# Performance work log

Measured on AMD Instinct MI355X. Metric: run time of the kernel, lower is better.

The kernel has to match this reference:

```python
import jax, jax.numpy as jnp
import numpy as np

N = 50000        # nodes
E = 1600000      # edges (before self loops)
IN = 128         # in_channels
HID = 32         # hidden_channels
HEADS = 4
OUT = 16         # out_channels
B = 512          # graphs in batch
NEG_SLOPE = 0.2  # PyG GATConv default


def _uniform(key, shape, fan_in):
    s = 1.0 / np.sqrt(fan_in)
    return jax.random.uniform(key, shape, jnp.float32, -s, s)


def setup_inputs() -> dict:
    key = jax.random.key(0)
    ks = jax.random.split(key, 12)
    x = jax.random.normal(ks[0], (N, IN), jnp.float32)
    edge_index = jax.random.randint(ks[1], (2, E), 0, N, dtype=jnp.int64)
    batch = jnp.sort(jax.random.randint(ks[2], (N,), 0, B, dtype=jnp.int64))
    return {
        "x": x,
        "edge_index": edge_index,
        "batch": batch,
        "W1": _uniform(ks[3], (IN, HEADS * HID), IN),
        "att_src": _uniform(ks[4], (HEADS, HID), HID),
        "att_dst": _uniform(ks[5], (HEADS, HID), HID),
        "b1": jnp.zeros((HEADS * HID,), jnp.float32),
        "lin1_w": _uniform(ks[6], (HEADS * HID, HID), HEADS * HID),
        "lin1_b": _uniform(ks[7], (HID,), HEADS * HID),
        "lin2_w": _uniform(ks[8], (HID, OUT), HID),
        "lin2_b": _uniform(ks[9], (OUT,), HID),
    }


def _gat_conv(x, src, dst, W1, att_src, att_dst, b1):
    # h: [N, H, C]
    h = (x @ W1).reshape(N, HEADS, HID)
    a_s = (h * att_src).sum(-1)   # [N, H]
    a_d = (h * att_dst).sum(-1)   # [N, H]
    # per-edge attention logits [E', H]
    alpha = jax.nn.leaky_relu(a_s[src] + a_d[dst], negative_slope=NEG_SLOPE)
    # segment softmax over incoming edges of each destination node
    amax = jax.lax.stop_gradient(jax.ops.segment_max(alpha, dst, num_segments=N))
    ex = jnp.exp(alpha - amax[dst])
    den = jax.ops.segment_sum(ex, dst, num_segments=N)
    a = ex / (den[dst] + 1e-16)
    # weighted scatter-aggregate of source features: [N, H, C]
    out = jax.ops.segment_sum(h[src] * a[:, :, None], dst, num_segments=N)
    return out.reshape(N, HEADS * HID) + b1


def reference(x, edge_index, batch, W1, att_src, att_dst, b1, lin1_w, lin1_b, lin2_w, lin2_b):
    # add self loops (PyG GATConv default add_self_loops=True)
    loop = jnp.arange(N, dtype=edge_index.dtype)
    src = jnp.concatenate([edge_index[0], loop])
    dst = jnp.concatenate([edge_index[1], loop])
    # dropout layers are identity in eval mode
    xh = jax.nn.elu(_gat_conv(x, src, dst, W1, att_src, att_dst, b1))
    g = jax.ops.segment_sum(xh, batch, num_segments=B)  # global_add_pool -> [B, H*C]
    g = g @ lin1_w + lin1_b
    return g @ lin2_w + lin2_b
```

## Files before the change

### kernel.cpp

```cpp
#include <hip/hip_runtime.h>
#include <hip/hip_bf16.h>
#include <hip/hip_fp16.h>

#define N_NODES 50000
#define E_EDGES 1600000
#define IN_CH 128
#define HID 32
#define HEADS 4
#define HC (HEADS * HID)
#define OUT_CH 16
#define B_GRAPHS 512
#define NEG_SLOPE 0.2f
#define CAP 96
#define NB 256
#define BNODES 196
#define PCAP 7168
#define ACHUNK 4096
#define APART 391
#define ROWS_PB 64
#define GEMM_BLOCKS 782

__device__ __forceinline__ unsigned short f2bf(float f) {
    unsigned int u = __float_as_uint(f);
    unsigned int r = (u + 0x7FFFu + ((u >> 16) & 1u)) >> 16;
    return (unsigned short)r;
}

__device__ __forceinline__ float lrelu_exp(float v) {
    v = v > 0.f ? v : NEG_SLOPE * v;
    return __expf(v);
}

__global__ __launch_bounds__(256) void k_fused(const float* __restrict__ x,
                                               const float* __restrict__ W1,
                                               const float* __restrict__ att_src,
                                               const float* __restrict__ att_dst,
                                               const int* __restrict__ ei,
                                               unsigned short* __restrict__ hb,
                                               float* __restrict__ a_s,
                                               float* __restrict__ a_d,
                                               int* __restrict__ gcur,
                                               unsigned int* __restrict__ ebuf,
                                               float* __restrict__ g) {
    __shared__ float smem[12288];
    const int t = threadIdx.x;

    if (blockIdx.x < APART) {
        int* scnt = (int*)smem;
        int* sbase = scnt + 4 * NB;
        const int wv = t >> 6;
        const int e0 = blockIdx.x * ACHUNK;
        int e1 = e0 + ACHUNK; if (e1 > E_EDGES) e1 = E_EDGES;
        for (int i = t; i < 4 * NB; i += 256) scnt[i] = 0;
        __syncthreads();
        const int* __restrict__ dstp = ei + E_EDGES;
        for (int e = e0 + t; e < e1; e += 256) {
            int d = dstp[e];
            atomicAdd(&scnt[wv * NB + d / BNODES], 1);
        }
        __syncthreads();
        if (t < NB) {
            int c0 = scnt[0 * NB + t], c1 = scnt[1 * NB + t];
            int c2 = scnt[2 * NB + t], c3 = scnt[3 * NB + t];
            int base = atomicAdd(&gcur[t], c0 + c1 + c2 + c3);
            sbase[0 * NB + t] = base;
            sbase[1 * NB + t] = base + c0;
            sbase[2 * NB + t] = base + c0 + c1;
            sbase[3 * NB + t] = base + c0 + c1 + c2;
            scnt[0 * NB + t] = 0; scnt[1 * NB + t] = 0;
            scnt[2 * NB + t] = 0; scnt[3 * NB + t] = 0;
        }
        __syncthreads();
        for (int e = e0 + t; e < e1; e += 256) {
            int d = dstp[e];
            int s = ei[e];
            int b = d / BNODES;
            int dl = d - b * BNODES;
            int pos = sbase[wv * NB + b] + atomicAdd(&scnt[wv * NB + b], 1);
            if (pos < PCAP)
                ebuf[(size_t)b * PCAP + pos] = ((unsigned int)dl << 16) | (unsigned int)s;
        }
        return;
    }

    float* sX = smem;
    float* sW = smem + 8192;
    const int bid = blockIdx.x - APART;
    const int n0 = bid * ROWS_PB;

    int gt = bid * 256 + t;
    if (gt < B_GRAPHS * HC) g[gt] = 0.f;

    for (int i = t; i < ROWS_PB * 32; i += 256) {
        int r = i >> 5, c4 = i & 31;
        int n = n0 + r;
        float4 v = (n < N_NODES) ? ((const float4*)x)[(size_t)n * 32 + c4]
                                 : make_float4(0.f, 0.f, 0.f, 0.f);
        ((float4*)sX)[i] = v;
    }

    float acc[8][4];
#pragma unroll
    for (int j = 0; j < 8; j++)
#pragma unroll
        for (int c = 0; c < 4; c++) acc[j][c] = 0.f;

    const int tx = t & 31;
    const int ty = t >> 5;

    for (int kb = 0; kb < 4; kb++) {
        __syncthreads();
        for (int i = t; i < 32 * 32; i += 256) {
            ((float4*)sW)[i] =
                ((const float4*)W1)[(size_t)(kb * 32 + (i >> 5)) * 32 + (i & 31)];
        }
        __syncthreads();
#pragma unroll
        for (int kk = 0; kk < 32; kk += 4) {
            float4 w0 = *(float4*)&sW[(kk + 0) * 128 + tx * 4];
            float4 w1 = *(float4*)&sW[(kk + 1) * 128 + tx * 4];
            float4 w2 = *(float4*)&sW[(kk + 2) * 128 + tx * 4];
            float4 w3 = *(float4*)&sW[(kk + 3) * 128 + tx * 4];
#pragma unroll
            for (int j = 0; j < 8; j++) {
                float4 xv = *(float4*)&sX[(ty * 8 + j) * 128 + kb * 32 + kk];
                acc[j][0] += xv.x * w0.x + xv.y * w1.x + xv.z * w2.x + xv.w * w3.x;
                acc[j][1] += xv.x * w0.y + xv.y * w1.y + xv.z * w2.y + xv.w * w3.y;
                acc[j][2] += xv.x * w0.z + xv.y * w1.z + xv.z * w2.z + xv.w * w3.z;
                acc[j][3] += xv.x * w0.w + xv.y * w1.w + xv.z * w2.w + xv.w * w3.w;
            }
        }
    }

#pragma unroll
    for (int j = 0; j < 8; j++) {
        int n = n0 + ty * 8 + j;
        if (n < N_NODES) {
            ushort4 o;
            o.x = f2bf(acc[j][0]); o.y = f2bf(acc[j][1]);
            o.z = f2bf(acc[j][2]); o.w = f2bf(acc[j][3]);
            *(ushort4*)&hb[(size_t)n * HC + tx * 4] = o;
        }
    }

    __syncthreads();
    float* sH = smem;
#pragma unroll
    for (int j = 0; j < 8; j++) {
        float* row = &sH[(ty * 8 + j) * 129 + tx * 4];
        row[0] = acc[j][0]; row[1] = acc[j][1];
        row[2] = acc[j][2]; row[3] = acc[j][3];
    }
    __syncthreads();
    if (t < 128) {
        int r = t & 63;
        int n = n0 + r;
        const float* __restrict__ av = (t < 64) ? att_src : att_dst;
        float s0 = 0.f, s1 = 0.f, s2 = 0.f, s3 = 0.f;
#pragma unroll 4
        for (int j = 0; j < 32; j++) {
            const float* row = &sH[r * 129 + j];
            s0 += row[0]  * av[j];
            s1 += row[32] * av[32 + j];
            s2 += row[64] * av[64 + j];
            s3 += row[96] * av[96 + j];
        }
        if (n < N_NODES) {
            float* dst = (t < 64) ? a_s : a_d;
            *(float4*)(dst + (size_t)n * 4) = make_float4(s0, s1, s2, s3);
        }
    }
}

#define NPW 13
__global__ __launch_bounds__(1024) void k_aggB(const unsigned int* __restrict__ ebuf,
                                               const int* __restrict__ gcur,
                                               const float* __restrict__ a_s,
                                               const float* __restrict__ a_d,
                                               const unsigned short* __restrict__ hb,
                                               const float* __restrict__ b1,
                                               const int* __restrict__ batch,
                                               float* __restrict__ g) {
    __shared__ unsigned short sbuf[BNODES * CAP];
    __shared__ int scnt[BNODES];
    __shared__ float sWt[16][4][97];
    const int t = threadIdx.x;
    const int b = blockIdx.x;
    const int dbase = b * BNODES;

    for (int i = t; i < BNODES; i += 1024) {
        int d = dbase + i;
        scnt[i] = (d < N_NODES) ? 1 : 0;
        sbuf[i * CAP] = (unsigned short)d;
    }
    __syncthreads();
    int m = gcur[b]; if (m > PCAP) m = PCAP;
    for (int i = t; i < m; i += 1024) {
        unsigned int p = ebuf[(size_t)b * PCAP + i];
        int dl = p >> 16;
        int s = p & 0xFFFFu;
        int c = atomicAdd(&scnt[dl], 1);
        if (c < CAP) sbuf[dl * CAP + c] = (unsigned short)s;
    }
    __syncthreads();

    const int wv = t >> 6;
    const int l = t & 63;
    const int head = l >> 4;
    const int c0 = 2 * l;
    int nl0 = wv * NPW;
    int nl1 = nl0 + NPW; if (nl1 > BNODES) nl1 = BNODES;
    int gn0 = dbase + nl0;
    if (gn0 >= N_NODES) return;
    int gn1 = dbase + nl1; if (gn1 > N_NODES) gn1 = N_NODES;
    const float2 bias = *(const float2*)(b1 + c0);
    float pool0 = 0.f, pool1 = 0.f;
    int cur = batch[gn0];
    for (int n = gn0; n < gn1; n++) {
        int bb = batch[n];
        if (bb != cur) {
            atomicAdd(&g[(size_t)cur * HC + c0], pool0);
            atomicAdd(&g[(size_t)cur * HC + c0 + 1], pool1);
            pool0 = pool1 = 0.f;
            cur = bb;
        }
        int nl = n - dbase;
        int c = scnt[nl]; if (c > CAP) c = CAP;
        float4 ad = *(const float4*)(a_d + (size_t)n * 4);
        const unsigned short* __restrict__ srow = &sbuf[nl * CAP];
        for (int i = l; i < c; i += 64) {
            int s = srow[i];
            float4 as = *(const float4*)(a_s + (size_t)s * 4);
            sWt[wv][0][i] = lrelu_exp(as.x + ad.x);
            sWt[wv][1][i] = lrelu_exp(as.y + ad.y);
            sWt[wv][2][i] = lrelu_exp(as.z + ad.z);
            sWt[wv][3][i] = lrelu_exp(as.w + ad.w);
        }
        __asm__ volatile("" ::: "memory");
        const float* __restrict__ wrow = &sWt[wv][head][0];
        float acc0 = 0.f, acc1 = 0.f, dsum = 0.f;
        int i = 0;
        for (; i + 4 <= c; i += 4) {
            int s0 = srow[i], s1 = srow[i + 1], s2 = srow[i + 2], s3 = srow[i + 3];
            float w0 = wrow[i], w1 = wrow[i + 1], w2 = wrow[i + 2], w3 = wrow[i + 3];
            unsigned int u0 = *(const unsigned int*)(hb + (size_t)s0 * HC + c0);
            unsigned int u1 = *(const unsigned int*)(hb + (size_t)s1 * HC + c0);
            unsigned int u2 = *(const unsigned int*)(hb + (size_t)s2 * HC + c0);
            unsigned int u3 = *(const unsigned int*)(hb + (size_t)s3 * HC + c0);
            dsum += (w0 + w1) + (w2 + w3);
            acc0 += w0 * __uint_as_float(u0 << 16) + w1 * __uint_as_float(u1 << 16)
                  + w2 * __uint_as_float(u2 << 16) + w3 * __uint_as_float(u3 << 16);
            acc1 += w0 * __uint_as_float(u0 & 0xFFFF0000u)
                  + w1 * __uint_as_float(u1 & 0xFFFF0000u)
                  + w2 * __uint_as_float(u2 & 0xFFFF0000u)
                  + w3 * __uint_as_float(u3 & 0xFFFF0000u);
        }
        for (; i < c; i++) {
            int s0 = srow[i];
            float w0 = wrow[i];
            unsigned int u0 = *(const unsigned int*)(hb + (size_t)s0 * HC + c0);
            dsum += w0;
            acc0 += w0 * __uint_as_float(u0 << 16);
            acc1 += w0 * __uint_as_float(u0 & 0xFFFF0000u);
        }
        __asm__ volatile("" ::: "memory");
        float inv = 1.f / (dsum + 1e-16f);
        float v0 = acc0 * inv + bias.x; v0 = v0 > 0.f ? v0 : (__expf(v0) - 1.f);
        float v1 = acc1 * inv + bias.y; v1 = v1 > 0.f ? v1 : (__expf(v1) - 1.f);
        pool0 += v0;
        pool1 += v1;
    }
    atomicAdd(&g[(size_t)cur * HC + c0], pool0);
    atomicAdd(&g[(size_t)cur * HC + c0 + 1], pool1);
}

__global__ __launch_bounds__(64) void k_mlp(const float* __restrict__ g,
                                            const float* __restrict__ w1,
                                            const float* __restrict__ bb1,
                                            const float* __restrict__ w2,
                                            const float* __restrict__ bb2,
                                            float* __restrict__ out) {
    __shared__ float sg[HC];
    __shared__ float st[HID];
    int b = blockIdx.x;
    int t = threadIdx.x;
    sg[t]      = g[(size_t)b * HC + t];
    sg[t + 64] = g[(size_t)b * HC + 64 + t];
    __syncthreads();
    if (t < HID) {
        float acc = bb1[t];
#pragma unroll 8
        for (int k = 0; k < HC; k++) acc += sg[k] * w1[(size_t)k * HID + t];
        st[t] = acc;
    }
    __syncthreads();
    if (t < OUT_CH) {
        float acc = bb2[t];
#pragma unroll
        for (int k = 0; k < HID; k++) acc += st[k] * w2[(size_t)k * OUT_CH + t];
        out[(size_t)b * OUT_CH + t] = acc;
    }
}

extern "C" void kernel_launch(void* const* d_in, const int* in_sizes, int n_in,
                              void* d_out, int out_size, void* d_ws, size_t ws_size,
                              hipStream_t stream) {
    const float* x       = (const float*)d_in[0];
    const int*   ei      = (const int*)d_in[1];
    const int*   batch   = (const int*)d_in[2];
    const float* W1      = (const float*)d_in[3];
    const float* att_src = (const float*)d_in[4];
    const float* att_dst = (const float*)d_in[5];
    const float* b1      = (const float*)d_in[6];
    const float* lin1_w  = (const float*)d_in[7];
    const float* lin1_b  = (const float*)d_in[8];
    const float* lin2_w  = (const float*)d_in[9];
    const float* lin2_b  = (const float*)d_in[10];
    float* out = (float*)d_out;

    float* ws = (float*)d_ws;
    unsigned short* hb   = (unsigned short*)ws;
    float*  a_s      = ws + 3200000;
    float*  a_d      = ws + 3400000;
    unsigned int* ebuf = (unsigned int*)(ws + 3600000);
    int*    gcur     = (int*)(ws + 5435008);
    float*  g        = ws + 5436000;

    hipMemsetAsync(gcur, 0, NB * sizeof(int), stream);

    k_fused<<<APART + GEMM_BLOCKS, 256, 0, stream>>>(
        x, W1, att_src, att_dst, ei, hb, a_s, a_d, gcur, ebuf, g);
    k_aggB<<<NB, 1024, 0, stream>>>(ebuf, gcur, a_s, a_d, hb, b1, batch, g);
    k_mlp<<<B_GRAPHS, 64, 0, stream>>>(g, lin1_w, lin1_b, lin2_w, lin2_b, out);
}
```

Before: 228.0 us.

## Shrink shared memory in GEMM and split aggregation buckets into sub-blocks

The fused GEMM now stages x one 32-column k-slice at a time in a padded buffer instead of the whole 64x128 tile. It also computes the attention dot products in two halves, which cuts its LDS footprint roughly in half so more blocks can be resident. The aggregation kernel is relaunched as four 256-thread blocks per bucket, each handling 49 destination nodes. Each of these blocks filters the shared bucket edge list, trading smaller blocks and higher occupancy for each block reading the full bucket segment.

```diff
diff --git a/kernel.cpp b/kernel.cpp
--- a/kernel.cpp
+++ b/kernel.cpp
@@ -14,11 +14,13 @@
 #define CAP 96
 #define NB 256
 #define BNODES 196
+#define BSUB 49
 #define PCAP 7168
 #define ACHUNK 4096
 #define APART 391
 #define ROWS_PB 64
 #define GEMM_BLOCKS 782
+#define SXS 33
 
 __device__ __forceinline__ unsigned short f2bf(float f) {
     unsigned int u = __float_as_uint(f);
@@ -42,7 +44,7 @@
                                                int* __restrict__ gcur,
                                                unsigned int* __restrict__ ebuf,
                                                float* __restrict__ g) {
-    __shared__ float smem[12288];
+    __shared__ float smem[6208];
     const int t = threadIdx.x;
 
     if (blockIdx.x < APART) {
@@ -84,21 +86,13 @@
     }
 
     float* sX = smem;
-    float* sW = smem + 8192;
+    float* sW = smem + 64 * SXS;
     const int bid = blockIdx.x - APART;
     const int n0 = bid * ROWS_PB;
 
     int gt = bid * 256 + t;
     if (gt < B_GRAPHS * HC) g[gt] = 0.f;
 
-    for (int i = t; i < ROWS_PB * 32; i += 256) {
-        int r = i >> 5, c4 = i & 31;
-        int n = n0 + r;
-        float4 v = (n < N_NODES) ? ((const float4*)x)[(size_t)n * 32 + c4]
-                                 : make_float4(0.f, 0.f, 0.f, 0.f);
-        ((float4*)sX)[i] = v;
-    }
-
     float acc[8][4];
 #pragma unroll
     for (int j = 0; j < 8; j++)
@@ -110,7 +104,15 @@
 
     for (int kb = 0; kb < 4; kb++) {
         __syncthreads();
-        for (int i = t; i < 32 * 32; i += 256) {
+        for (int i = t; i < 512; i += 256) {
+            int r = i >> 3, c4 = i & 7;
+            int n = n0 + r;
+            float4 v = (n < N_NODES)
+                ? ((const float4*)x)[(size_t)n * 32 + kb * 8 + c4]
+                : make_float4(0.f, 0.f, 0.f, 0.f);
+            *(float4*)&sX[r * SXS + c4 * 4] = v;
+        }
+        for (int i = t; i < 1024; i += 256) {
             ((float4*)sW)[i] =
                 ((const float4*)W1)[(size_t)(kb * 32 + (i >> 5)) * 32 + (i & 31)];
         }
@@ -123,7 +125,7 @@
             float4 w3 = *(float4*)&sW[(kk + 3) * 128 + tx * 4];
 #pragma unroll
             for (int j = 0; j < 8; j++) {
-                float4 xv = *(float4*)&sX[(ty * 8 + j) * 128 + kb * 32 + kk];
+                float4 xv = *(float4*)&sX[(ty * 8 + j) * SXS + kk];
                 acc[j][0] += xv.x * w0.x + xv.y * w1.x + xv.z * w2.x + xv.w * w3.x;
                 acc[j][1] += xv.x * w0.y + xv.y * w1.y + xv.z * w2.y + xv.w * w3.y;
                 acc[j][2] += xv.x * w0.z + xv.y * w1.z + xv.z * w2.z + xv.w * w3.z;
@@ -143,64 +145,73 @@
         }
     }
 
-    __syncthreads();
     float* sH = smem;
-#pragma unroll
-    for (int j = 0; j < 8; j++) {
-        float* row = &sH[(ty * 8 + j) * 129 + tx * 4];
-        row[0] = acc[j][0]; row[1] = acc[j][1];
-        row[2] = acc[j][2]; row[3] = acc[j][3];
-    }
-    __syncthreads();
-    if (t < 128) {
-        int r = t & 63;
-        int n = n0 + r;
-        const float* __restrict__ av = (t < 64) ? att_src : att_dst;
-        float s0 = 0.f, s1 = 0.f, s2 = 0.f, s3 = 0.f;
+    for (int half = 0; half < 2; half++) {
+        __syncthreads();
+        if ((ty >> 2) == half) {
+            int rbase = (ty & 3) * 8;
+#pragma unroll
+            for (int j = 0; j < 8; j++) {
+                float* row = &sH[(rbase + j) * 129 + tx * 4];
+                row[0] = acc[j][0]; row[1] = acc[j][1];
+                row[2] = acc[j][2]; row[3] = acc[j][3];
+            }
+        }
+        __syncthreads();
+        if (t < 64) {
+            int r = t & 31;
+            int n = n0 + half * 32 + r;
+            const float* __restrict__ av = (t < 32) ? att_src : att_dst;
+            float s0 = 0.f, s1 = 0.f, s2 = 0.f, s3 = 0.f;
 #pragma unroll 4
-        for (int j = 0; j < 32; j++) {
-            const float* row = &sH[r * 129 + j];
-            s0 += row[0]  * av[j];
-            s1 += row[32] * av[32 + j];
-            s2 += row[64] * av[64 + j];
-            s3 += row[96] * av[96 + j];
-        }
-        if (n < N_NODES) {
-            float* dst = (t < 64) ? a_s : a_d;
-            *(float4*)(dst + (size_t)n * 4) = make_float4(s0, s1, s2, s3);
+            for (int j = 0; j < 32; j++) {
+                const float* row = &sH[r * 129 + j];
+                s0 += row[0]  * av[j];
+                s1 += row[32] * av[32 + j];
+                s2 += row[64] * av[64 + j];
+                s3 += row[96] * av[96 + j];
+            }
+            if (n < N_NODES) {
+                float* dst = (t < 32) ? a_s : a_d;
+                *(float4*)(dst + (size_t)n * 4) = make_float4(s0, s1, s2, s3);
+            }
         }
     }
 }
 
 #define NPW 13
-__global__ __launch_bounds__(1024) void k_aggB(const unsigned int* __restrict__ ebuf,
-                                               const int* __restrict__ gcur,
-                                               const float* __restrict__ a_s,
-                                               const float* __restrict__ a_d,
-                                               const unsigned short* __restrict__ hb,
-                                               const float* __restrict__ b1,
-                                               const int* __restrict__ batch,
-                                               float* __restrict__ g) {
-    __shared__ unsigned short sbuf[BNODES * CAP];
-    __shared__ int scnt[BNODES];
-    __shared__ float sWt[16][4][97];
+__global__ __launch_bounds__(256) void k_aggB(const unsigned int* __restrict__ ebuf,
+                                              const int* __restrict__ gcur,
+                                              const float* __restrict__ a_s,
+                                              const float* __restrict__ a_d,
+                                              const unsigned short* __restrict__ hb,
+                                              const float* __restrict__ b1,
+                                              const int* __restrict__ batch,
+                                              float* __restrict__ g) {
+    __shared__ unsigned short sbuf[BSUB * CAP];
+    __shared__ int scnt[BSUB];
+    __shared__ float sWt[4][4][97];
     const int t = threadIdx.x;
-    const int b = blockIdx.x;
-    const int dbase = b * BNODES;
-
-    for (int i = t; i < BNODES; i += 1024) {
+    const int bucket = blockIdx.x >> 2;
+    const int sub = blockIdx.x & 3;
+    const int l0 = sub * BSUB;
+    const int dbase = bucket * BNODES + l0;
+
+    for (int i = t; i < BSUB; i += 256) {
         int d = dbase + i;
         scnt[i] = (d < N_NODES) ? 1 : 0;
         sbuf[i * CAP] = (unsigned short)d;
     }
     __syncthreads();
-    int m = gcur[b]; if (m > PCAP) m = PCAP;
-    for (int i = t; i < m; i += 1024) {
-        unsigned int p = ebuf[(size_t)b * PCAP + i];
-        int dl = p >> 16;
-        int s = p & 0xFFFFu;
-        int c = atomicAdd(&scnt[dl], 1);
-        if (c < CAP) sbuf[dl * CAP + c] = (unsigned short)s;
+    int m = gcur[bucket]; if (m > PCAP) m = PCAP;
+    const unsigned int* __restrict__ seg = ebuf + (size_t)bucket * PCAP;
+    for (int i = t; i < m; i += 256) {
+        unsigned int p = seg[i];
+        int dl = (int)(p >> 16) - l0;
+        if ((unsigned)dl < BSUB) {
+            int c = atomicAdd(&scnt[dl], 1);
+            if (c < CAP) sbuf[dl * CAP + c] = (unsigned short)(p & 0xFFFFu);
+        }
     }
     __syncthreads();
 
@@ -209,9 +220,9 @@
     const int head = l >> 4;
     const int c0 = 2 * l;
     int nl0 = wv * NPW;
-    int nl1 = nl0 + NPW; if (nl1 > BNODES) nl1 = BNODES;
+    int nl1 = nl0 + NPW; if (nl1 > BSUB) nl1 = BSUB;
     int gn0 = dbase + nl0;
-    if (gn0 >= N_NODES) return;
+    if (gn0 >= N_NODES || nl0 >= BSUB) return;
     int gn1 = dbase + nl1; if (gn1 > N_NODES) gn1 = N_NODES;
     const float2 bias = *(const float2*)(b1 + c0);
     float pool0 = 0.f, pool1 = 0.f;
@@ -330,6 +341,6 @@
 
     k_fused<<<APART + GEMM_BLOCKS, 256, 0, stream>>>(
         x, W1, att_src, att_dst, ei, hb, a_s, a_d, gcur, ebuf, g);
-    k_aggB<<<NB, 1024, 0, stream>>>(ebuf, gcur, a_s, a_d, hb, b1, batch, g);
+    k_aggB<<<NB * 4, 256, 0, stream>>>(ebuf, gcur, a_s, a_d, hb, b1, batch, g);
     k_mlp<<<B_GRAPHS, 64, 0, stream>>>(g, lin1_w, lin1_b, lin2_w, lin2_b, out);
 }
```

Result: slower. 325.0 us (+42.5%).
